# Performance work log

Hardware: AMD Instinct MI355X
Metric: run time of the kernel (lower is better)

## Reference

```python
import math
import jax, jax.numpy as jnp
import numpy as np

N, T, D, H, DH = 4, 2048, 1024, 16, 64
CAP = 30.0
EPS = 1e-5


def _layernorm(x, g, b):
    m = jnp.mean(x, axis=-1, keepdims=True)
    v = jnp.mean(jnp.square(x - m), axis=-1, keepdims=True)
    return (x - m) * jax.lax.rsqrt(v + EPS) * g + b


def _rope(x):
    # x: [N, H, t, d]; interleaved rotary (rotary-embedding-torch style), theta=10000
    t, d = x.shape[2], x.shape[3]
    inv_freq = 1.0 / (10000.0 ** (jnp.arange(0, d, 2, dtype=jnp.float32) / d))
    ang = jnp.arange(t, dtype=jnp.float32)[:, None] * inv_freq[None, :]  # [t, d/2]
    cos, sin = jnp.cos(ang), jnp.sin(ang)
    x1, x2 = x[..., 0::2], x[..., 1::2]
    r1 = x1 * cos - x2 * sin
    r2 = x1 * sin + x2 * cos
    return jnp.stack([r1, r2], axis=-1).reshape(x.shape)


def setup_inputs() -> dict:
    key = jax.random.key(0)
    ks = jax.random.split(key, 8)
    s = 0.02
    lengths = jax.random.randint(ks[6], (N,), T // 2, T + 1).astype(jnp.int32)
    key_padding_mask = jnp.arange(T)[None, :] >= lengths[:, None]  # True = pad
    attn_mask = jnp.triu(jnp.ones((T, T), dtype=bool), 1)  # causal: True = masked
    return {
        "x": jax.random.normal(ks[0], (N, T, D), jnp.float32),
        "ln_g": jnp.ones((D,), jnp.float32),
        "ln_b": jnp.zeros((D,), jnp.float32),
        "Wq": jax.random.normal(ks[1], (D, H * DH), jnp.float32) * s,
        "bq": jnp.zeros((H * DH,), jnp.float32),
        "Wk": jax.random.normal(ks[2], (D, H * DH), jnp.float32) * s,
        "bk": jnp.zeros((H * DH,), jnp.float32),
        "Wv": jax.random.normal(ks[3], (D, H * DH), jnp.float32) * s,
        "bv": jnp.zeros((H * DH,), jnp.float32),
        "Wo": jax.random.normal(ks[4], (H * DH, D), jnp.float32) * s,
        "bo": jnp.zeros((D,), jnp.float32),
        "key_padding_mask": key_padding_mask,
        "attn_mask": attn_mask,
        "key_value_sequence_lengths": lengths,
    }


def reference(x, ln_g, ln_b, Wq, bq, Wk, bk, Wv, bv, Wo, bo,
              key_padding_mask, attn_mask, key_value_sequence_lengths):
    n, t, _ = x.shape
    h = _layernorm(x, ln_g, ln_b)  # shared LN for q/k/v (self-attention)
    q = (h @ Wq + bq).reshape(n, t, H, DH).transpose(0, 2, 1, 3)  # [n,H,t,d]
    k = (h @ Wk + bk).reshape(n, t, H, DH).transpose(0, 2, 1, 3)
    v = (h @ Wv + bv).reshape(n, t, H, DH).transpose(0, 2, 1, 3)
    q = _rope(q)
    k = _rope(k)
    scores = jnp.einsum('bhtd,bhTd->bhtT', q, k) / math.sqrt(DH)
    scores = CAP * jnp.tanh(scores / CAP)  # tanh soft-cap
    mask = key_padding_mask[:, None, None, :] | attn_mask[None, None, :, :]
    scores = jnp.where(mask, -jnp.inf, scores)
    attn = jax.nn.softmax(scores, axis=-1)
    out = jnp.einsum('bhtT,bhTd->bhtd', attn, v)
    out = out.transpose(0, 2, 1, 3).reshape(n, t, H * DH)
    return out @ Wo + bo
```

## Files before the change

kernel.cpp:

```cpp
#include <hip/hip_runtime.h>
#include <hip/hip_bf16.h>

typedef unsigned short u16;
typedef unsigned int   u32;
typedef __bf16 bf16x8 __attribute__((ext_vector_type(8)));
typedef float  f32x4  __attribute__((ext_vector_type(4)));

#define NB 4
#define T_ 2048
#define D_ 1024
#define H_ 16
#define DH 64
#define M_ (NB * T_)
#define PSTR 72

__device__ __forceinline__ float bf2f(u16 u) {
    union { u32 i; float f; } v; v.i = ((u32)u) << 16; return v.f;
}
__device__ __forceinline__ u16 f2bf(float f) {
    union { float fl; u32 i; } v; v.fl = f;
    u32 r = v.i + 0x7fff + ((v.i >> 16) & 1);
    return (u16)(r >> 16);
}

__device__ __forceinline__ void gl_lds16(const u16* g, u16* l) {
    __builtin_amdgcn_global_load_lds((const __attribute__((address_space(1))) void*)g,
                                     (__attribute__((address_space(3))) void*)l,
                                     16, 0, 0);
}

__device__ __forceinline__ int detect_f32(const u16* p) {
    int weird = 0;
    const int lane = threadIdx.x & 63;
    #pragma unroll
    for (int i = 0; i < 4; ++i) {
        const u16 u = p[lane * 4 + i];
        const int e = (u >> 7) & 0xFF;
        weird += (e == 0xFF || (e >= 0x01 && e <= 0x3F) || (e >= 0xC0 && e <= 0xFE));
    }
    #pragma unroll
    for (int off = 32; off; off >>= 1) weird += __shfl_xor(weird, off);
    return weird >= 16;
}

__device__ __forceinline__ int read_len(const void* raw, int b) {
    const int* a32 = (const int*)raw;
    bool ok32 = true;
    #pragma unroll
    for (int i = 0; i < NB; ++i) {
        const int v = a32[i];
        if (v < 1 || v > T_) ok32 = false;
    }
    int v = ok32 ? a32[b] : (int)((const long long*)raw)[b];
    return min(max(v, 1), T_);
}

__global__ __launch_bounds__(256) void prep_kernel(const void* __restrict__ xraw,
                                                   const void* __restrict__ graw,
                                                   const void* __restrict__ braw,
                                                   u16* __restrict__ h,
                                                   const void* __restrict__ W0,
                                                   const void* __restrict__ W1,
                                                   const void* __restrict__ W2,
                                                   const void* __restrict__ W3,
                                                   u16* __restrict__ Wt0,
                                                   u16* __restrict__ Wt1,
                                                   u16* __restrict__ Wt2,
                                                   u16* __restrict__ Wt3,
                                                   float2* __restrict__ tab,
                                                   u32* __restrict__ ctr) {
    __shared__ __align__(16) u16 sh[64 * PSTR];
    const int bid = blockIdx.x;
    const int tid = threadIdx.x;

    if (bid < M_) {
        const int row = bid;
        const int isf = detect_f32((const u16*)xraw);
        float* red = (float*)sh;

        float xv[4];
        if (isf) {
            const float* xr = (const float*)xraw + (size_t)row * D_;
            *(float4*)xv = *(const float4*)&xr[tid * 4];
        } else {
            const u16* xr = (const u16*)xraw + (size_t)row * D_;
            u16 loc[4] __attribute__((aligned(8)));
            *(uint2*)loc = *(const uint2*)&xr[tid * 4];
            #pragma unroll
            for (int i = 0; i < 4; ++i) xv[i] = bf2f(loc[i]);
        }

        float s = xv[0] + xv[1] + xv[2] + xv[3];
        float q = xv[0]*xv[0] + xv[1]*xv[1] + xv[2]*xv[2] + xv[3]*xv[3];
        #pragma unroll
        for (int off = 32; off; off >>= 1) {
            s += __shfl_xor(s, off);
            q += __shfl_xor(q, off);
        }
        const int wave = tid >> 6, lane = tid & 63;
        if (lane == 0) { red[wave] = s; red[4 + wave] = q; }
        __syncthreads();
        s = red[0] + red[1] + red[2] + red[3];
        q = red[4] + red[5] + red[6] + red[7];

        const float mean = s * (1.0f / D_);
        const float var  = q * (1.0f / D_) - mean * mean;
        const float rs   = rsqrtf(var + 1e-5f);

        u16 o[4] __attribute__((aligned(8)));
        #pragma unroll
        for (int i = 0; i < 4; ++i) {
            const int c = tid * 4 + i;
            const float gv = isf ? ((const float*)graw)[c] : bf2f(((const u16*)graw)[c]);
            const float bv = isf ? ((const float*)braw)[c] : bf2f(((const u16*)braw)[c]);
            o[i] = f2bf((xv[i] - mean) * rs * gv + bv);
        }
        *(uint2*)&h[(size_t)row * D_ + tid * 4] = *(uint2*)o;
    } else if (bid < M_ + 1024) {
        const int w = bid - M_;
        const int z = w >> 8;
        const int t = w & 255;
        const void* Wraw = (z == 0) ? W0 : (z == 1) ? W1 : (z == 2) ? W2 : W3;
        u16* Wt          = (z == 0) ? Wt0 : (z == 1) ? Wt1 : (z == 2) ? Wt2 : Wt3;
        u16 (*tile)[PSTR] = (u16(*)[PSTR])sh;
        const int isf = detect_f32((const u16*)Wraw);
        const int n0 = (t & 15) * 64;
        const int k0 = (t >> 4) * 64;
        const int tr  = tid >> 2;
        const int tc  = (tid & 3) * 16;

        if (isf) {
            const float* W = (const float*)Wraw;
            #pragma unroll
            for (int i = 0; i < 16; ++i)
                tile[tc + i][tr] = f2bf(W[(size_t)(k0 + tr) * D_ + n0 + tc + i]);
        } else {
            const u16* W = (const u16*)Wraw;
            #pragma unroll
            for (int i = 0; i < 16; ++i)
                tile[tc + i][tr] = W[(size_t)(k0 + tr) * D_ + n0 + tc + i];
        }
        __syncthreads();
        *(uint4*)&Wt[(size_t)(n0 + tr) * D_ + k0 + tc]     = *(uint4*)&tile[tr][tc];
        *(uint4*)&Wt[(size_t)(n0 + tr) * D_ + k0 + tc + 8] = *(uint4*)&tile[tr][tc + 8];
    } else {
        const int gid = (bid - (M_ + 1024)) * 256 + tid;
        if (gid == 0 && ctr) ctr[0] = 0;
        const int t = gid >> 5, i = gid & 31;
        const float inv = exp2f(-(float)i * 0.41524101186092f);
        const float ang = (float)t * inv;
        float sv, cv;
        sincosf(ang, &sv, &cv);
        tab[gid] = make_float2(cv, sv);
    }
}

__global__ __launch_bounds__(256) void wconv_kernel(const void* __restrict__ Wraw,
                                                    u16* __restrict__ Wt) {
    __shared__ u16 tile[64][PSTR];
    const int isf = detect_f32((const u16*)Wraw);
    const int n0 = blockIdx.x * 64;
    const int k0 = blockIdx.y * 64;
    const int tid = threadIdx.x;
    const int tr  = tid >> 2;
    const int tc  = (tid & 3) * 16;

    if (isf) {
        const float* W = (const float*)Wraw;
        #pragma unroll
        for (int i = 0; i < 16; ++i)
            tile[tc + i][tr] = f2bf(W[(size_t)(k0 + tr) * D_ + n0 + tc + i]);
    } else {
        const u16* W = (const u16*)Wraw;
        #pragma unroll
        for (int i = 0; i < 16; ++i)
            tile[tc + i][tr] = W[(size_t)(k0 + tr) * D_ + n0 + tc + i];
    }
    __syncthreads();
    *(uint4*)&Wt[(size_t)(n0 + tr) * D_ + k0 + tc]     = *(uint4*)&tile[tr][tc];
    *(uint4*)&Wt[(size_t)(n0 + tr) * D_ + k0 + tc + 8] = *(uint4*)&tile[tr][tc + 8];
}

__global__ __launch_bounds__(256) void vtrans_kernel(const u16* __restrict__ vtmp,
                                                     u16* __restrict__ vt) {
    __shared__ u16 tile[64][PSTR];
    const int bh = blockIdx.y;
    const int b  = bh >> 4;
    const int hh = bh & 15;
    const int t0 = blockIdx.x * 64;
    const int tid = threadIdx.x;
    const int tr  = tid >> 2;
    const int tc  = (tid & 3) * 16;

    #pragma unroll
    for (int i = 0; i < 16; ++i)
        tile[tc + i][tr] = vtmp[(size_t)(b * T_ + t0 + tr) * D_ + hh * DH + tc + i];
    __syncthreads();
    u16* dst = vt + (size_t)bh * DH * T_ + (size_t)tr * T_ + t0;
    *(uint4*)&dst[tc]     = *(uint4*)&tile[tr][tc];
    *(uint4*)&dst[tc + 8] = *(uint4*)&tile[tr][tc + 8];
}

__global__ __launch_bounds__(256) void qkv_kernel(const u16* __restrict__ A,
                                                  const u16* __restrict__ Wt3,
                                                  const void* __restrict__ Braw,
                                                  const void* __restrict__ bqr,
                                                  const void* __restrict__ bkr,
                                                  const void* __restrict__ bvr,
                                                  u16* __restrict__ qo,
                                                  u16* __restrict__ ko,
                                                  u16* __restrict__ vo,
                                                  const float2* __restrict__ tab) {
    __shared__ __align__(16) u16 As[128 * 64];
    __shared__ __align__(16) u16 Bs[128 * 64];

    const int tid   = threadIdx.x;
    const int wave  = tid >> 6;
    const int lane  = tid & 63;
    const int quad  = lane >> 4;
    const int lr    = lane & 15;

    const int bid = blockIdx.x;
    const int wg  = (bid & 7) * 192 + (bid >> 3);
    const int ntile = (wg % 24) * 128;
    const int mtile = (wg / 24) * 128;
    const int seg   = ntile >> 10;

    const int isf = detect_f32((const u16*)Braw);

    const int srow = wave * 8 + (lane >> 3);
    const int sc   = (((lane & 7) ^ (lane >> 3)) * 8);
    const u16* aP = A   + (size_t)(mtile + srow) * D_ + sc;
    const u16* bP = Wt3 + (size_t)(ntile + srow) * D_ + sc;
    u16* aL = As + (wave * 8) * 64;
    u16* bL = Bs + (wave * 8) * 64;

    const int mbase = (wave >> 1) * 64;
    const int nbase = (wave & 1) * 64;

    f32x4 acc[4][4];
    #pragma unroll
    for (int m = 0; m < 4; ++m)
        #pragma unroll
        for (int n = 0; n < 4; ++n)
            acc[m][n] = (f32x4){0.f, 0.f, 0.f, 0.f};

    for (int k0 = 0; k0 < D_; k0 += 64) {
        #pragma unroll
        for (int j = 0; j < 4; ++j) {
            gl_lds16(aP + (size_t)(j * 32) * D_ + k0, aL + (j * 32) * 64);
            gl_lds16(bP + (size_t)(j * 32) * D_ + k0, bL + (j * 32) * 64);
        }
        __syncthreads();

        #pragma unroll
        for (int c = 0; c < 2; ++c) {
            bf16x8 af[4], bfr[4];
            #pragma unroll
            for (int m = 0; m < 4; ++m) {
                const int row = mbase + m * 16 + lr;
                af[m] = *(const bf16x8*)&As[row * 64 + (((c << 2) | quad) ^ (row & 7)) * 8];
            }
            #pragma unroll
            for (int n = 0; n < 4; ++n) {
                const int row = nbase + n * 16 + lr;
                bfr[n] = *(const bf16x8*)&Bs[row * 64 + (((c << 2) | quad) ^ (row & 7)) * 8];
            }
            #pragma unroll
            for (int m = 0; m < 4; ++m)
                #pragma unroll
                for (int n = 0; n < 4; ++n)
                    acc[m][n] = __builtin_amdgcn_mfma_f32_16x16x32_bf16(af[m], bfr[n], acc[m][n], 0, 0, 0);
        }
        __syncthreads();
    }

    const void* biasraw = (seg == 0) ? bqr : (seg == 1) ? bkr : bvr;
    u16* out            = (seg == 0) ? qo  : (seg == 1) ? ko  : vo;
    const int nloc = (ntile & 1023) + nbase;

    #pragma unroll
    for (int m = 0; m < 4; ++m) {
        #pragma unroll
        for (int n = 0; n < 4; ++n) {
            const int ncl = nloc + n * 16 + lr;
            const float bv = isf ? ((const float*)biasraw)[ncl]
                                 : bf2f(((const u16*)biasraw)[ncl]);
            #pragma unroll
            for (int r = 0; r < 4; ++r) {
                const int mrow = mtile + mbase + m * 16 + quad * 4 + r;
                float v = acc[m][n][r] + bv;
                if (seg < 2) {
                    const float other = __shfl_xor(v, 1);
                    const int d = ncl & (DH - 1);
                    const int t = mrow & (T_ - 1);
                    const float2 cs = tab[t * 32 + (d >> 1)];
                    v = (d & 1) ? (other * cs.y + v * cs.x) : (v * cs.x - other * cs.y);
                }
                out[(size_t)mrow * D_ + ncl] = f2bf(v);
            }
        }
    }
}

__global__ __launch_bounds__(256) void gemm128_kernel(const u16* __restrict__ A,
                                                      const u16* __restrict__ Bt,
                                                      const void* __restrict__ Braw,
                                                      const void* __restrict__ biasraw,
                                                      void* __restrict__ out,
                                                      const int nx,
                                                      const int mode) {
    __shared__ __align__(16) u16 As[128 * 64];
    __shared__ __align__(16) u16 Bs[128 * 64];

    const int tid   = threadIdx.x;
    const int wave  = tid >> 6;
    const int lane  = tid & 63;
    const int quad  = lane >> 4;
    const int lr    = lane & 15;

    const int bid = blockIdx.x;
    const int cpx = (nx * (M_ / 128)) >> 3;
    const int wg  = (bid & 7) * cpx + (bid >> 3);
    const int ntile = (wg % nx) * 128;
    const int mtile = (wg / nx) * 128;

    const int isf = detect_f32((const u16*)Braw);

    const int srow = wave * 8 + (lane >> 3);
    const int sc   = (((lane & 7) ^ (lane >> 3)) * 8);
    const u16* aP = A  + (size_t)(mtile + srow) * D_ + sc;
    const u16* bP = Bt + (size_t)(ntile + srow) * D_ + sc;
    u16* aL = As + (wave * 8) * 64;
    u16* bL = Bs + (wave * 8) * 64;

    const int mbase = (wave >> 1) * 64;
    const int nbase = (wave & 1) * 64;

    f32x4 acc[4][4];
    #pragma unroll
    for (int m = 0; m < 4; ++m)
        #pragma unroll
        for (int n = 0; n < 4; ++n)
            acc[m][n] = (f32x4){0.f, 0.f, 0.f, 0.f};

    for (int k0 = 0; k0 < D_; k0 += 64) {
        #pragma unroll
        for (int j = 0; j < 4; ++j) {
            gl_lds16(aP + (size_t)(j * 32) * D_ + k0, aL + (j * 32) * 64);
            gl_lds16(bP + (size_t)(j * 32) * D_ + k0, bL + (j * 32) * 64);
        }
        __syncthreads();

        #pragma unroll
        for (int c = 0; c < 2; ++c) {
            bf16x8 af[4], bfr[4];
            #pragma unroll
            for (int m = 0; m < 4; ++m) {
                const int row = mbase + m * 16 + lr;
                af[m] = *(const bf16x8*)&As[row * 64 + (((c << 2) | quad) ^ (row & 7)) * 8];
            }
            #pragma unroll
            for (int n = 0; n < 4; ++n) {
                const int row = nbase + n * 16 + lr;
                bfr[n] = *(const bf16x8*)&Bs[row * 64 + (((c << 2) | quad) ^ (row & 7)) * 8];
            }
            #pragma unroll
            for (int m = 0; m < 4; ++m)
                #pragma unroll
                for (int n = 0; n < 4; ++n)
                    acc[m][n] = __builtin_amdgcn_mfma_f32_16x16x32_bf16(af[m], bfr[n], acc[m][n], 0, 0, 0);
        }
        __syncthreads();
    }

    #pragma unroll
    for (int m = 0; m < 4; ++m) {
        #pragma unroll
        for (int n = 0; n < 4; ++n) {
            const int ncol = ntile + nbase + n * 16 + lr;
            const float bv = isf ? ((const float*)biasraw)[ncol]
                                 : bf2f(((const u16*)biasraw)[ncol]);
            #pragma unroll
            for (int r = 0; r < 4; ++r) {
                const int mrow = mtile + mbase + m * 16 + quad * 4 + r;
                float v = acc[m][n][r] + bv;
                if (mode == 2) {
                    const float other = __shfl_xor(v, 1);
                    const int d = ncol & (DH - 1);
                    const int t = mrow & (T_ - 1);
                    const int i = d >> 1;
                    const float inv = exp2f(-(float)i * 0.41524101186092f);
                    const float ang = (float)t * inv;
                    float sv, cv;
                    __sincosf(ang, &sv, &cv);
                    v = (d & 1) ? (other * sv + v * cv) : (v * cv - other * sv);
                }
                const int d  = ncol & (DH - 1);
                const int hh = ncol >> 6;
                const int t  = mrow & (T_ - 1);
                const int bb = mrow >> 11;
                if (mode == 0) {
                    if (isf) ((float*)out)[(size_t)mrow * D_ + ncol] = v;
                    else     ((u16*)out)[(size_t)mrow * D_ + ncol] = f2bf(v);
                } else if (mode == 1) {
                    ((u16*)out)[(((size_t)(bb * H_ + hh) * DH) + d) * T_ + t] = f2bf(v);
                } else {
                    ((u16*)out)[(((size_t)(bb * H_ + hh) * T_) + t) * DH + d] = f2bf(v);
                }
            }
        }
    }
}

__global__ __launch_bounds__(256) void gemm_kernel(const u16* __restrict__ A,
                                                   const void* __restrict__ Braw,
                                                   const void* __restrict__ biasraw,
                                                   void* __restrict__ out,
                                                   const int mode) {
    __shared__ __align__(16) u16 As[128 * 32];
    __shared__ __align__(16) u16 Bs[64 * 32];

    const int tid   = threadIdx.x;
    const int ntile = blockIdx.x * 64;
    const int mtile = blockIdx.y * 128;
    const int wave  = tid >> 6;
    const int lane  = tid & 63;
    const int quad  = lane >> 4;
    const int lr    = lane & 15;

    const int isf = detect_f32((const u16*)Braw);
    const float* Bf = (const float*)Braw;
    const u16*   Bu = (const u16*)Braw;

    f32x4 acc[2][4];
    #pragma unroll
    for (int s = 0; s < 2; ++s)
        #pragma unroll
        for (int n = 0; n < 4; ++n)
            acc[s][n] = (f32x4){0.f, 0.f, 0.f, 0.f};

    const int ar  = tid >> 1;
    const int akb = (tid & 1) * 16;
    const int bn  = tid & 63;
    const int bkb = (tid >> 6) * 8;
    const u16* Arow = A + (size_t)(mtile + ar) * D_ + akb;
    const size_t bcol0 = (size_t)bkb * D_ + ntile + bn;

    for (int k0 = 0; k0 < D_; k0 += 32) {
        *(uint4*)&As[ar * 32 + akb]     = *(const uint4*)(Arow + k0);
        *(uint4*)&As[ar * 32 + akb + 8] = *(const uint4*)(Arow + k0 + 8);
        {
            u16 tmp[8] __attribute__((aligned(16)));
            if (isf) {
                #pragma unroll
                for (int j = 0; j < 8; ++j) tmp[j] = f2bf(Bf[bcol0 + (size_t)(k0 + j) * D_]);
            } else {
                #pragma unroll
                for (int j = 0; j < 8; ++j) tmp[j] = Bu[bcol0 + (size_t)(k0 + j) * D_];
            }
            *(uint4*)&Bs[bn * 32 + bkb] = *(uint4*)tmp;
        }
        __syncthreads();

        const int mbase = wave * 32;
        bf16x8 af0 = *(const bf16x8*)&As[(mbase +      lr) * 32 + quad * 8];
        bf16x8 af1 = *(const bf16x8*)&As[(mbase + 16 + lr) * 32 + quad * 8];
        #pragma unroll
        for (int nt = 0; nt < 4; ++nt) {
            bf16x8 bf = *(const bf16x8*)&Bs[(nt * 16 + lr) * 32 + quad * 8];
            acc[0][nt] = __builtin_amdgcn_mfma_f32_16x16x32_bf16(af0, bf, acc[0][nt], 0, 0, 0);
            acc[1][nt] = __builtin_amdgcn_mfma_f32_16x16x32_bf16(af1, bf, acc[1][nt], 0, 0, 0);
        }
        __syncthreads();
    }

    #pragma unroll
    for (int s2 = 0; s2 < 2; ++s2) {
        #pragma unroll
        for (int nt = 0; nt < 4; ++nt) {
            const int ncol = ntile + nt * 16 + lr;
            const float bv = isf ? ((const float*)biasraw)[ncol]
                                 : bf2f(((const u16*)biasraw)[ncol]);
            #pragma unroll
            for (int r = 0; r < 4; ++r) {
                const int mrow = mtile + wave * 32 + s2 * 16 + quad * 4 + r;
                float v = acc[s2][nt][r] + bv;
                if (mode == 2) {
                    const float other = __shfl_xor(v, 1);
                    const int d = ncol & (DH - 1);
                    const int t = mrow & (T_ - 1);
                    const int i = d >> 1;
                    const float inv = exp2f(-(float)i * 0.41524101186092f);
                    const float ang = (float)t * inv;
                    const float cv = cosf(ang), sv = sinf(ang);
                    v = (d & 1) ? (other * sv + v * cv) : (v * cv - other * sv);
                }
                const int d  = ncol & (DH - 1);
                const int hh = ncol >> 6;
                const int t  = mrow & (T_ - 1);
                const int bb = mrow >> 11;
                if (mode == 0) {
                    if (isf) ((float*)out)[(size_t)mrow * D_ + ncol] = v;
                    else     ((u16*)out)[(size_t)mrow * D_ + ncol] = f2bf(v);
                } else if (mode == 1) {
                    ((u16*)out)[(((size_t)(bb * H_ + hh) * DH) + d) * T_ + t] = f2bf(v);
                } else {
                    ((u16*)out)[(((size_t)(bb * H_ + hh) * T_) + t) * DH + d] = f2bf(v);
                }
            }
        }
    }
}

__global__ __launch_bounds__(256) void attn_kernel(const u16* __restrict__ Q,
                                                   const u16* __restrict__ K,
                                                   const u16* __restrict__ Vt,
                                                   const void* __restrict__ lensraw,
                                                   u16* __restrict__ ctx,
                                                   u32* __restrict__ ctr,
                                                   const int rowmajor) {
    __shared__ __align__(16) u16 Ps[64 * PSTR];
    __shared__ __align__(16) u16 Ks[64 * PSTR];
    __shared__ __align__(16) u16 Vts[64 * PSTR];
    __shared__ int item_s;

    const int tid  = threadIdx.x;
    const int wave = tid >> 6;
    const int lane = tid & 63;
    const int quad = lane >> 4;
    const int lr   = lane & 15;
    const int srow = tid >> 2;
    const int scb  = (tid & 3) * 16;
    const int prow = wave * 16 + quad * 4;

    const float C1 = 1.44269504f / 120.0f;
    const float C2 = -60.0f * 1.44269504f;

    for (int iter = 0; ; ++iter) {
        if (tid == 0)
            item_s = ctr ? (int)atomicAdd(ctr, 1u)
                         : (iter == 0 ? (int)blockIdx.x : NB * H_ * 32);
        __syncthreads();
        const int item = item_s;
        if (item >= NB * H_ * 32) break;

        const int qt = 31 - (item >> 6);
        const int bh = item & 63;
        const int qs = qt * 64;
        const int b  = bh >> 4;
        const int hh = bh & 15;
        const int len = read_len(lensraw, b);

        const size_t qkstride = rowmajor ? (size_t)D_ : (size_t)DH;
        const size_t qkoff    = rowmajor ? ((size_t)b * T_ * D_ + hh * DH)
                                         : ((size_t)bh * T_ * DH);
        const u16* Qp = Q + qkoff;
        const u16* Kp = K + qkoff;
        const u16* Vb = Vt + (size_t)bh * DH * T_;

        *(uint4*)&Ps[srow * PSTR + scb]     = *(const uint4*)&Qp[(size_t)(qs + srow) * qkstride + scb];
        *(uint4*)&Ps[srow * PSTR + scb + 8] = *(const uint4*)&Qp[(size_t)(qs + srow) * qkstride + scb + 8];
        const bf16x8 qa0 = *(const bf16x8*)&Ps[(wave * 16 + lr) * PSTR + quad * 8];
        const bf16x8 qa1 = *(const bf16x8*)&Ps[(wave * 16 + lr) * PSTR + 32 + quad * 8];
        {
            uint4 k0 = *(const uint4*)&Kp[(size_t)srow * qkstride + scb];
            uint4 k1 = *(const uint4*)&Kp[(size_t)srow * qkstride + scb + 8];
            uint4 v0 = *(const uint4*)&Vb[(size_t)srow * T_ + scb];
            uint4 v1 = *(const uint4*)&Vb[(size_t)srow * T_ + scb + 8];
            *(uint4*)&Ks[srow * PSTR + scb]      = k0;
            *(uint4*)&Ks[srow * PSTR + scb + 8]  = k1;
            *(uint4*)&Vts[srow * PSTR + scb]     = v0;
            *(uint4*)&Vts[srow * PSTR + scb + 8] = v1;
        }
        __syncthreads();

        f32x4 acc[4];
        float l_loc[4] = {0.f, 0.f, 0.f, 0.f};
        #pragma unroll
        for (int nt = 0; nt < 4; ++nt) acc[nt] = (f32x4){0.f, 0.f, 0.f, 0.f};

        const int ktn = min(qs + 63, len - 1) / 64 + 1;

        uint4 kr0, kr1, vr0, vr1;
        for (int kt = 0; kt < ktn; ++kt) {
            const int ks = kt * 64;
            const bool havenext = (kt + 1 < ktn);

            if (havenext) {
                const int ns = ks + 64;
                kr0 = *(const uint4*)&Kp[(size_t)(ns + srow) * qkstride + scb];
                kr1 = *(const uint4*)&Kp[(size_t)(ns + srow) * qkstride + scb + 8];
                vr0 = *(const uint4*)&Vb[(size_t)srow * T_ + ns + scb];
                vr1 = *(const uint4*)&Vb[(size_t)srow * T_ + ns + scb + 8];
            }

            f32x4 s[4];
            #pragma unroll
            for (int nt = 0; nt < 4; ++nt) s[nt] = (f32x4){0.f, 0.f, 0.f, 0.f};
            __builtin_amdgcn_s_setprio(1);
            #pragma unroll
            for (int nt = 0; nt < 4; ++nt) {
                bf16x8 kb0 = *(const bf16x8*)&Ks[(nt * 16 + lr) * PSTR + quad * 8];
                bf16x8 kb1 = *(const bf16x8*)&Ks[(nt * 16 + lr) * PSTR + 32 + quad * 8];
                s[nt] = __builtin_amdgcn_mfma_f32_16x16x32_bf16(qa0, kb0, s[nt], 0, 0, 0);
                s[nt] = __builtin_amdgcn_mfma_f32_16x16x32_bf16(qa1, kb1, s[nt], 0, 0, 0);
            }
            __builtin_amdgcn_s_setprio(0);

            const bool need_mask = (ks == qs) || (ks + 63 >= len);
            if (!need_mask) {
                #pragma unroll
                for (int r = 0; r < 4; ++r) {
                    #pragma unroll
                    for (int nt = 0; nt < 4; ++nt) {
                        const float z = __builtin_amdgcn_exp2f(s[nt][r] * C1);
                        const float p = __builtin_amdgcn_exp2f(C2 * __builtin_amdgcn_rcpf(z + 1.0f));
                        l_loc[r] += p;
                        Ps[(prow + r) * PSTR + nt * 16 + lr] = f2bf(p);
                    }
                }
            } else {
                #pragma unroll
                for (int r = 0; r < 4; ++r) {
                    const int trow = qs + prow + r;
                    #pragma unroll
                    for (int nt = 0; nt < 4; ++nt) {
                        const float z = __builtin_amdgcn_exp2f(s[nt][r] * C1);
                        float p = __builtin_amdgcn_exp2f(C2 * __builtin_amdgcn_rcpf(z + 1.0f));
                        const int col = ks + nt * 16 + lr;
                        p = (col > trow || col >= len) ? 0.f : p;
                        l_loc[r] += p;
                        Ps[(prow + r) * PSTR + nt * 16 + lr] = f2bf(p);
                    }
                }
            }

            bf16x8 pa0 = *(const bf16x8*)&Ps[(wave * 16 + lr) * PSTR + quad * 8];
            bf16x8 pa1 = *(const bf16x8*)&Ps[(wave * 16 + lr) * PSTR + 32 + quad * 8];
            __builtin_amdgcn_s_setprio(1);
            #pragma unroll
            for (int nt = 0; nt < 4; ++nt) {
                bf16x8 vb0 = *(const bf16x8*)&Vts[(nt * 16 + lr) * PSTR + quad * 8];
                bf16x8 vb1 = *(const bf16x8*)&Vts[(nt * 16 + lr) * PSTR + 32 + quad * 8];
                acc[nt] = __builtin_amdgcn_mfma_f32_16x16x32_bf16(pa0, vb0, acc[nt], 0, 0, 0);
                acc[nt] = __builtin_amdgcn_mfma_f32_16x16x32_bf16(pa1, vb1, acc[nt], 0, 0, 0);
            }
            __builtin_amdgcn_s_setprio(0);

            if (havenext) {
                __syncthreads();
                *(uint4*)&Ks[srow * PSTR + scb]      = kr0;
                *(uint4*)&Ks[srow * PSTR + scb + 8]  = kr1;
                *(uint4*)&Vts[srow * PSTR + scb]     = vr0;
                *(uint4*)&Vts[srow * PSTR + scb + 8] = vr1;
                __syncthreads();
            }
        }

        #pragma unroll
        for (int r = 0; r < 4; ++r) {
            float l = l_loc[r];
            #pragma unroll
            for (int off = 1; off < 16; off <<= 1) l += __shfl_xor(l, off);
            const float invl = (l > 0.f) ? (1.0f / l) : 0.f;
            const int qrow = prow + r;
            #pragma unroll
            for (int nt = 0; nt < 4; ++nt) {
                ctx[(size_t)(b * T_ + qs + qrow) * D_ + hh * DH + nt * 16 + lr] =
                    f2bf(acc[nt][r] * invl);
            }
        }
    }
}

extern "C" void kernel_launch(void* const* d_in, const int* in_sizes, int n_in,
                              void* d_out, int out_size, void* d_ws, size_t ws_size,
                              hipStream_t stream) {
    u16* h = (u16*)d_ws;
    const size_t MD = (size_t)M_ * D_;
    const size_t WD = (size_t)D_ * D_;
    u16* q  = h + MD;
    u16* k  = q + MD;
    u16* vt = k + MD;
    const bool havewt  = ws_size >= (4 * MD + 4 * WD) * sizeof(u16);
    const bool havebig = ws_size >= (5 * MD + 4 * WD) * sizeof(u16)
                                    + (size_t)T_ * 32 * sizeof(float2) + 64;
    u16* wtq = havewt ? (vt + MD)  : nullptr;
    u16* wtk = havewt ? (wtq + WD) : nullptr;
    u16* wtv = havewt ? (wtk + WD) : nullptr;
    u16* wto = havewt ? (wtv + WD) : nullptr;
    u16* vtmp = havebig ? (wto + WD) : nullptr;
    float2* tab = havebig ? (float2*)(vtmp + MD) : nullptr;
    u32* ctr = havebig ? (u32*)(tab + (size_t)T_ * 32) : nullptr;

    if (havebig) {
        prep_kernel<<<M_ + 1024 + 256, 256, 0, stream>>>(
            d_in[0], d_in[1], d_in[2], h,
            d_in[3], d_in[5], d_in[7], d_in[9], wtq, wtk, wtv, wto, tab, ctr);

        qkv_kernel<<<1536, 256, 0, stream>>>(
            h, wtq, d_in[3], d_in[4], d_in[6], d_in[8], q, k, vtmp, tab);

        vtrans_kernel<<<dim3(T_ / 64, NB * H_), 256, 0, stream>>>(vtmp, vt);

        attn_kernel<<<1024, 256, 0, stream>>>(q, k, vt, d_in[13], h, ctr, 1);

        gemm128_kernel<<<8 * (M_ / 128), 256, 0, stream>>>(
            h, wto, d_in[9], d_in[10], d_out, 8, 0);
    } else if (havewt) {
        prep_kernel<<<M_, 256, 0, stream>>>(
            d_in[0], d_in[1], d_in[2], h,
            d_in[3], d_in[5], d_in[7], d_in[9], wtq, wtk, wtv, wto, nullptr, nullptr);
        dim3 wgrid(D_ / 64, D_ / 64);
        wconv_kernel<<<wgrid, 256, 0, stream>>>(d_in[3], wtq);
        wconv_kernel<<<wgrid, 256, 0, stream>>>(d_in[5], wtk);
        wconv_kernel<<<wgrid, 256, 0, stream>>>(d_in[7], wtv);
        wconv_kernel<<<wgrid, 256, 0, stream>>>(d_in[9], wto);

        const int g1 = 8 * (M_ / 128);
        gemm128_kernel<<<g1, 256, 0, stream>>>(h, wtq, d_in[3], d_in[4], q, 8, 2);
        gemm128_kernel<<<g1, 256, 0, stream>>>(h, wtk, d_in[5], d_in[6], k, 8, 2);
        gemm128_kernel<<<g1, 256, 0, stream>>>(h, wtv, d_in[7], d_in[8], vt, 8, 1);

        attn_kernel<<<NB * H_ * 32, 256, 0, stream>>>(q, k, vt, d_in[13], h, nullptr, 0);

        gemm128_kernel<<<g1, 256, 0, stream>>>(h, wto, d_in[9], d_in[10], d_out, 8, 0);
    } else {
        prep_kernel<<<M_, 256, 0, stream>>>(
            d_in[0], d_in[1], d_in[2], h,
            d_in[3], d_in[5], d_in[7], d_in[9], nullptr, nullptr, nullptr, nullptr, nullptr, nullptr);
        dim3 ggrid(D_ / 64, M_ / 128);
        gemm_kernel<<<ggrid, 256, 0, stream>>>(h, d_in[3], d_in[4], q, 2);
        gemm_kernel<<<ggrid, 256, 0, stream>>>(h, d_in[5], d_in[6], k, 2);
        gemm_kernel<<<ggrid, 256, 0, stream>>>(h, d_in[7], d_in[8], vt, 1);

        attn_kernel<<<NB * H_ * 32, 256, 0, stream>>>(q, k, vt, d_in[13], h, nullptr, 0);

        gemm_kernel<<<ggrid, 256, 0, stream>>>(h, d_in[9], d_in[10], d_out, 0);
    }
}
```

Measured before the change: 360.5 us.

## Double-buffer GEMM K-loop and enlarge QKV tile to 256x256

```diff
diff --git a/kernel.cpp b/kernel.cpp
--- a/kernel.cpp
+++ b/kernel.cpp
@@ -201,86 +201,94 @@
     *(uint4*)&dst[tc + 8] = *(uint4*)&tile[tr][tc + 8];
 }
 
-__global__ __launch_bounds__(256) void qkv_kernel(const u16* __restrict__ A,
-                                                  const u16* __restrict__ Wt3,
-                                                  const void* __restrict__ Braw,
-                                                  const void* __restrict__ bqr,
-                                                  const void* __restrict__ bkr,
-                                                  const void* __restrict__ bvr,
-                                                  u16* __restrict__ qo,
-                                                  u16* __restrict__ ko,
-                                                  u16* __restrict__ vo,
-                                                  const float2* __restrict__ tab) {
-    __shared__ __align__(16) u16 As[128 * 64];
-    __shared__ __align__(16) u16 Bs[128 * 64];
-
-    const int tid   = threadIdx.x;
-    const int wave  = tid >> 6;
-    const int lane  = tid & 63;
-    const int quad  = lane >> 4;
-    const int lr    = lane & 15;
+__global__ __launch_bounds__(512) void qkv256_kernel(const u16* __restrict__ A,
+                                                     const u16* __restrict__ Wt3,
+                                                     const void* __restrict__ Braw,
+                                                     const void* __restrict__ bqr,
+                                                     const void* __restrict__ bkr,
+                                                     const void* __restrict__ bvr,
+                                                     u16* __restrict__ qo,
+                                                     u16* __restrict__ ko,
+                                                     u16* __restrict__ vo,
+                                                     const float2* __restrict__ tab) {
+    __shared__ __align__(16) u16 As[2][256 * 32];
+    __shared__ __align__(16) u16 Bs[2][256 * 32];
+
+    const int tid  = threadIdx.x;
+    const int wave = tid >> 6;
+    const int lane = tid & 63;
+    const int quad = lane >> 4;
+    const int lr   = lane & 15;
+    const int wr   = wave >> 2;
+    const int wc   = wave & 3;
 
     const int bid = blockIdx.x;
-    const int wg  = (bid & 7) * 192 + (bid >> 3);
-    const int ntile = (wg % 24) * 128;
-    const int mtile = (wg / 24) * 128;
+    const int wg  = (bid & 7) * 48 + (bid >> 3);
+    const int ntile = (wg % 12) * 256;
+    const int mtile = (wg / 12) * 256;
     const int seg   = ntile >> 10;
 
     const int isf = detect_f32((const u16*)Braw);
 
-    const int srow = wave * 8 + (lane >> 3);
-    const int sc   = (((lane & 7) ^ (lane >> 3)) * 8);
-    const u16* aP = A   + (size_t)(mtile + srow) * D_ + sc;
-    const u16* bP = Wt3 + (size_t)(ntile + srow) * D_ + sc;
-    u16* aL = As + (wave * 8) * 64;
-    u16* bL = Bs + (wave * 8) * 64;
-
-    const int mbase = (wave >> 1) * 64;
-    const int nbase = (wave & 1) * 64;
-
-    f32x4 acc[4][4];
-    #pragma unroll
-    for (int m = 0; m < 4; ++m)
+    const int srow = wave * 16 + (lane >> 2);
+    const int scol = (lane & 3) * 8;
+    const u16* aP0 = A   + (size_t)(mtile + srow) * D_ + scol;
+    const u16* aP1 = A   + (size_t)(mtile + 128 + srow) * D_ + scol;
+    const u16* bP0 = Wt3 + (size_t)(ntile + srow) * D_ + scol;
+    const u16* bP1 = Wt3 + (size_t)(ntile + 128 + srow) * D_ + scol;
+    const int lo0 = (wave * 16) * 32;
+    const int lo1 = (128 + wave * 16) * 32;
+
+    f32x4 acc[8][4];
+    #pragma unroll
+    for (int m = 0; m < 8; ++m)
         #pragma unroll
         for (int n = 0; n < 4; ++n)
             acc[m][n] = (f32x4){0.f, 0.f, 0.f, 0.f};
 
-    for (int k0 = 0; k0 < D_; k0 += 64) {
-        #pragma unroll
-        for (int j = 0; j < 4; ++j) {
-            gl_lds16(aP + (size_t)(j * 32) * D_ + k0, aL + (j * 32) * 64);
-            gl_lds16(bP + (size_t)(j * 32) * D_ + k0, bL + (j * 32) * 64);
-        }
+    gl_lds16(aP0, &As[0][lo0]);
+    gl_lds16(aP1, &As[0][lo1]);
+    gl_lds16(bP0, &Bs[0][lo0]);
+    gl_lds16(bP1, &Bs[0][lo1]);
+    __syncthreads();
+
+    int cur = 0;
+    for (int kk = 0; kk < D_ / 32; ++kk) {
+        const int nxt = cur ^ 1;
+        if (kk + 1 < D_ / 32) {
+            const int k0 = (kk + 1) * 32;
+            gl_lds16(aP0 + k0, &As[nxt][lo0]);
+            gl_lds16(aP1 + k0, &As[nxt][lo1]);
+            gl_lds16(bP0 + k0, &Bs[nxt][lo0]);
+            gl_lds16(bP1 + k0, &Bs[nxt][lo1]);
+        }
+
+        bf16x8 af[8], bfr[4];
+        #pragma unroll
+        for (int m = 0; m < 8; ++m)
+            af[m] = *(const bf16x8*)&As[cur][(wr * 128 + m * 16 + lr) * 32 + quad * 8];
+        #pragma unroll
+        for (int n = 0; n < 4; ++n)
+            bfr[n] = *(const bf16x8*)&Bs[cur][(wc * 64 + n * 16 + lr) * 32 + quad * 8];
+
+        __builtin_amdgcn_s_setprio(1);
+        #pragma unroll
+        for (int m = 0; m < 8; ++m)
+            #pragma unroll
+            for (int n = 0; n < 4; ++n)
+                acc[m][n] = __builtin_amdgcn_mfma_f32_16x16x32_bf16(af[m], bfr[n], acc[m][n], 0, 0, 0);
+        __builtin_amdgcn_s_setprio(0);
+
         __syncthreads();
-
-        #pragma unroll
-        for (int c = 0; c < 2; ++c) {
-            bf16x8 af[4], bfr[4];
-            #pragma unroll
-            for (int m = 0; m < 4; ++m) {
-                const int row = mbase + m * 16 + lr;
-                af[m] = *(const bf16x8*)&As[row * 64 + (((c << 2) | quad) ^ (row & 7)) * 8];
-            }
-            #pragma unroll
-            for (int n = 0; n < 4; ++n) {
-                const int row = nbase + n * 16 + lr;
-                bfr[n] = *(const bf16x8*)&Bs[row * 64 + (((c << 2) | quad) ^ (row & 7)) * 8];
-            }
-            #pragma unroll
-            for (int m = 0; m < 4; ++m)
-                #pragma unroll
-                for (int n = 0; n < 4; ++n)
-                    acc[m][n] = __builtin_amdgcn_mfma_f32_16x16x32_bf16(af[m], bfr[n], acc[m][n], 0, 0, 0);
-        }
-        __syncthreads();
+        cur = nxt;
     }
 
     const void* biasraw = (seg == 0) ? bqr : (seg == 1) ? bkr : bvr;
     u16* out            = (seg == 0) ? qo  : (seg == 1) ? ko  : vo;
-    const int nloc = (ntile & 1023) + nbase;
-
-    #pragma unroll
-    for (int m = 0; m < 4; ++m) {
+    const int nloc = (ntile & 1023) + wc * 64;
+
+    #pragma unroll
+    for (int m = 0; m < 8; ++m) {
         #pragma unroll
         for (int n = 0; n < 4; ++n) {
             const int ncl = nloc + n * 16 + lr;
@@ -288,7 +296,7 @@
                                  : bf2f(((const u16*)biasraw)[ncl]);
             #pragma unroll
             for (int r = 0; r < 4; ++r) {
-                const int mrow = mtile + mbase + m * 16 + quad * 4 + r;
+                const int mrow = mtile + wr * 128 + m * 16 + quad * 4 + r;
                 float v = acc[m][n][r] + bv;
                 if (seg < 2) {
                     const float other = __shfl_xor(v, 1);
@@ -310,8 +318,8 @@
                                                       void* __restrict__ out,
                                                       const int nx,
                                                       const int mode) {
-    __shared__ __align__(16) u16 As[128 * 64];
-    __shared__ __align__(16) u16 Bs[128 * 64];
+    __shared__ __align__(16) u16 As[2][128 * 32];
+    __shared__ __align__(16) u16 Bs[2][128 * 32];
 
     const int tid   = threadIdx.x;
     const int wave  = tid >> 6;
@@ -327,12 +335,14 @@
 
     const int isf = detect_f32((const u16*)Braw);
 
-    const int srow = wave * 8 + (lane >> 3);
-    const int sc   = (((lane & 7) ^ (lane >> 3)) * 8);
-    const u16* aP = A  + (size_t)(mtile + srow) * D_ + sc;
-    const u16* bP = Bt + (size_t)(ntile + srow) * D_ + sc;
-    u16* aL = As + (wave * 8) * 64;
-    u16* bL = Bs + (wave * 8) * 64;
+    const int srow = wave * 16 + (lane >> 2);
+    const int scol = (lane & 3) * 8;
+    const u16* aP0 = A  + (size_t)(mtile + srow) * D_ + scol;
+    const u16* aP1 = A  + (size_t)(mtile + 64 + srow) * D_ + scol;
+    const u16* bP0 = Bt + (size_t)(ntile + srow) * D_ + scol;
+    const u16* bP1 = Bt + (size_t)(ntile + 64 + srow) * D_ + scol;
+    const int lo0 = (wave * 16) * 32;
+    const int lo1 = (64 + wave * 16) * 32;
 
     const int mbase = (wave >> 1) * 64;
     const int nbase = (wave & 1) * 64;
@@ -344,34 +354,41 @@
         for (int n = 0; n < 4; ++n)
             acc[m][n] = (f32x4){0.f, 0.f, 0.f, 0.f};
 
-    for (int k0 = 0; k0 < D_; k0 += 64) {
-        #pragma unroll
-        for (int j = 0; j < 4; ++j) {
-            gl_lds16(aP + (size_t)(j * 32) * D_ + k0, aL + (j * 32) * 64);
-            gl_lds16(bP + (size_t)(j * 32) * D_ + k0, bL + (j * 32) * 64);
-        }
+    gl_lds16(aP0, &As[0][lo0]);
+    gl_lds16(aP1, &As[0][lo1]);
+    gl_lds16(bP0, &Bs[0][lo0]);
+    gl_lds16(bP1, &Bs[0][lo1]);
+    __syncthreads();
+
+    int cur = 0;
+    for (int kk = 0; kk < D_ / 32; ++kk) {
+        const int nxt = cur ^ 1;
+        if (kk + 1 < D_ / 32) {
+            const int k0 = (kk + 1) * 32;
+            gl_lds16(aP0 + k0, &As[nxt][lo0]);
+            gl_lds16(aP1 + k0, &As[nxt][lo1]);
+            gl_lds16(bP0 + k0, &Bs[nxt][lo0]);
+            gl_lds16(bP1 + k0, &Bs[nxt][lo1]);
+        }
+
+        bf16x8 af[4], bfr[4];
+        #pragma unroll
+        for (int m = 0; m < 4; ++m)
+            af[m] = *(const bf16x8*)&As[cur][(mbase + m * 16 + lr) * 32 + quad * 8];
+        #pragma unroll
+        for (int n = 0; n < 4; ++n)
+            bfr[n] = *(const bf16x8*)&Bs[cur][(nbase + n * 16 + lr) * 32 + quad * 8];
+
+        __builtin_amdgcn_s_setprio(1);
+        #pragma unroll
+        for (int m = 0; m < 4; ++m)
+            #pragma unroll
+            for (int n = 0; n < 4; ++n)
+                acc[m][n] = __builtin_amdgcn_mfma_f32_16x16x32_bf16(af[m], bfr[n], acc[m][n], 0, 0, 0);
+        __builtin_amdgcn_s_setprio(0);
+
         __syncthreads();
-
-        #pragma unroll
-        for (int c = 0; c < 2; ++c) {
-            bf16x8 af[4], bfr[4];
-            #pragma unroll
-            for (int m = 0; m < 4; ++m) {
-                const int row = mbase + m * 16 + lr;
-                af[m] = *(const bf16x8*)&As[row * 64 + (((c << 2) | quad) ^ (row & 7)) * 8];
-            }
-            #pragma unroll
-            for (int n = 0; n < 4; ++n) {
-                const int row = nbase + n * 16 + lr;
-                bfr[n] = *(const bf16x8*)&Bs[row * 64 + (((c << 2) | quad) ^ (row & 7)) * 8];
-            }
-            #pragma unroll
-            for (int m = 0; m < 4; ++m)
-                #pragma unroll
-                for (int n = 0; n < 4; ++n)
-                    acc[m][n] = __builtin_amdgcn_mfma_f32_16x16x32_bf16(af[m], bfr[n], acc[m][n], 0, 0, 0);
-        }
-        __syncthreads();
+        cur = nxt;
     }
 
     #pragma unroll
@@ -699,7 +716,7 @@
             d_in[0], d_in[1], d_in[2], h,
             d_in[3], d_in[5], d_in[7], d_in[9], wtq, wtk, wtv, wto, tab, ctr);
 
-        qkv_kernel<<<1536, 256, 0, stream>>>(
+        qkv256_kernel<<<384, 512, 0, stream>>>(
             h, wtq, d_in[3], d_in[4], d_in[6], d_in[8], q, k, vtmp, tab);
 
         vtrans_kernel<<<dim3(T_ / 64, NB * H_), 256, 0, stream>>>(vtmp, vt);
```

After: 397.4 us. 1.1x slower.

## Double-buffer LDS tiles in QKV and output GEMMs to overlap loads with MFMA

Applied to the files above, without the earlier changes.

```diff
diff --git a/kernel.cpp b/kernel.cpp
--- a/kernel.cpp
+++ b/kernel.cpp
@@ -211,8 +211,8 @@
                                                   u16* __restrict__ ko,
                                                   u16* __restrict__ vo,
                                                   const float2* __restrict__ tab) {
-    __shared__ __align__(16) u16 As[128 * 64];
-    __shared__ __align__(16) u16 Bs[128 * 64];
+    __shared__ __align__(16) u16 As[2][128 * 64];
+    __shared__ __align__(16) u16 Bs[2][128 * 64];
 
     const int tid   = threadIdx.x;
     const int wave  = tid >> 6;
@@ -232,8 +232,7 @@
     const int sc   = (((lane & 7) ^ (lane >> 3)) * 8);
     const u16* aP = A   + (size_t)(mtile + srow) * D_ + sc;
     const u16* bP = Wt3 + (size_t)(ntile + srow) * D_ + sc;
-    u16* aL = As + (wave * 8) * 64;
-    u16* bL = Bs + (wave * 8) * 64;
+    const int lofs = (wave * 8) * 64;
 
     const int mbase = (wave >> 1) * 64;
     const int nbase = (wave & 1) * 64;
@@ -245,13 +244,24 @@
         for (int n = 0; n < 4; ++n)
             acc[m][n] = (f32x4){0.f, 0.f, 0.f, 0.f};
 
-    for (int k0 = 0; k0 < D_; k0 += 64) {
-        #pragma unroll
-        for (int j = 0; j < 4; ++j) {
-            gl_lds16(aP + (size_t)(j * 32) * D_ + k0, aL + (j * 32) * 64);
-            gl_lds16(bP + (size_t)(j * 32) * D_ + k0, bL + (j * 32) * 64);
-        }
-        __syncthreads();
+    #pragma unroll
+    for (int j = 0; j < 4; ++j) {
+        gl_lds16(aP + (size_t)(j * 32) * D_, &As[0][lofs + (j * 32) * 64]);
+        gl_lds16(bP + (size_t)(j * 32) * D_, &Bs[0][lofs + (j * 32) * 64]);
+    }
+    __syncthreads();
+
+    int cur = 0;
+    for (int kk = 0; kk < D_ / 64; ++kk) {
+        const int nxt = cur ^ 1;
+        if (kk + 1 < D_ / 64) {
+            const int k0 = (kk + 1) * 64;
+            #pragma unroll
+            for (int j = 0; j < 4; ++j) {
+                gl_lds16(aP + (size_t)(j * 32) * D_ + k0, &As[nxt][lofs + (j * 32) * 64]);
+                gl_lds16(bP + (size_t)(j * 32) * D_ + k0, &Bs[nxt][lofs + (j * 32) * 64]);
+            }
+        }
 
         #pragma unroll
         for (int c = 0; c < 2; ++c) {
@@ -259,20 +269,24 @@
             #pragma unroll
             for (int m = 0; m < 4; ++m) {
                 const int row = mbase + m * 16 + lr;
-                af[m] = *(const bf16x8*)&As[row * 64 + (((c << 2) | quad) ^ (row & 7)) * 8];
+                af[m] = *(const bf16x8*)&As[cur][row * 64 + (((c << 2) | quad) ^ (row & 7)) * 8];
             }
             #pragma unroll
             for (int n = 0; n < 4; ++n) {
                 const int row = nbase + n * 16 + lr;
-                bfr[n] = *(const bf16x8*)&Bs[row * 64 + (((c << 2) | quad) ^ (row & 7)) * 8];
-            }
+                bfr[n] = *(const bf16x8*)&Bs[cur][row * 64 + (((c << 2) | quad) ^ (row & 7)) * 8];
+            }
+            __builtin_amdgcn_s_setprio(1);
             #pragma unroll
             for (int m = 0; m < 4; ++m)
                 #pragma unroll
                 for (int n = 0; n < 4; ++n)
                     acc[m][n] = __builtin_amdgcn_mfma_f32_16x16x32_bf16(af[m], bfr[n], acc[m][n], 0, 0, 0);
-        }
+            __builtin_amdgcn_s_setprio(0);
+        }
+
         __syncthreads();
+        cur = nxt;
     }
 
     const void* biasraw = (seg == 0) ? bqr : (seg == 1) ? bkr : bvr;
@@ -310,8 +324,8 @@
                                                       void* __restrict__ out,
                                                       const int nx,
                                                       const int mode) {
-    __shared__ __align__(16) u16 As[128 * 64];
-    __shared__ __align__(16) u16 Bs[128 * 64];
+    __shared__ __align__(16) u16 As[2][128 * 64];
+    __shared__ __align__(16) u16 Bs[2][128 * 64];
 
     const int tid   = threadIdx.x;
     const int wave  = tid >> 6;
@@ -331,8 +345,7 @@
     const int sc   = (((lane & 7) ^ (lane >> 3)) * 8);
     const u16* aP = A  + (size_t)(mtile + srow) * D_ + sc;
     const u16* bP = Bt + (size_t)(ntile + srow) * D_ + sc;
-    u16* aL = As + (wave * 8) * 64;
-    u16* bL = Bs + (wave * 8) * 64;
+    const int lofs = (wave * 8) * 64;
 
     const int mbase = (wave >> 1) * 64;
     const int nbase = (wave & 1) * 64;
@@ -344,13 +357,24 @@
         for (int n = 0; n < 4; ++n)
             acc[m][n] = (f32x4){0.f, 0.f, 0.f, 0.f};
 
-    for (int k0 = 0; k0 < D_; k0 += 64) {
-        #pragma unroll
-        for (int j = 0; j < 4; ++j) {
-            gl_lds16(aP + (size_t)(j * 32) * D_ + k0, aL + (j * 32) * 64);
-            gl_lds16(bP + (size_t)(j * 32) * D_ + k0, bL + (j * 32) * 64);
-        }
-        __syncthreads();
+    #pragma unroll
+    for (int j = 0; j < 4; ++j) {
+        gl_lds16(aP + (size_t)(j * 32) * D_, &As[0][lofs + (j * 32) * 64]);
+        gl_lds16(bP + (size_t)(j * 32) * D_, &Bs[0][lofs + (j * 32) * 64]);
+    }
+    __syncthreads();
+
+    int cur = 0;
+    for (int kk = 0; kk < D_ / 64; ++kk) {
+        const int nxt = cur ^ 1;
+        if (kk + 1 < D_ / 64) {
+            const int k0 = (kk + 1) * 64;
+            #pragma unroll
+            for (int j = 0; j < 4; ++j) {
+                gl_lds16(aP + (size_t)(j * 32) * D_ + k0, &As[nxt][lofs + (j * 32) * 64]);
+                gl_lds16(bP + (size_t)(j * 32) * D_ + k0, &Bs[nxt][lofs + (j * 32) * 64]);
+            }
+        }
 
         #pragma unroll
         for (int c = 0; c < 2; ++c) {
@@ -358,20 +382,24 @@
             #pragma unroll
             for (int m = 0; m < 4; ++m) {
                 const int row = mbase + m * 16 + lr;
-                af[m] = *(const bf16x8*)&As[row * 64 + (((c << 2) | quad) ^ (row & 7)) * 8];
+                af[m] = *(const bf16x8*)&As[cur][row * 64 + (((c << 2) | quad) ^ (row & 7)) * 8];
             }
             #pragma unroll
             for (int n = 0; n < 4; ++n) {
                 const int row = nbase + n * 16 + lr;
-                bfr[n] = *(const bf16x8*)&Bs[row * 64 + (((c << 2) | quad) ^ (row & 7)) * 8];
-            }
+                bfr[n] = *(const bf16x8*)&Bs[cur][row * 64 + (((c << 2) | quad) ^ (row & 7)) * 8];
+            }
+            __builtin_amdgcn_s_setprio(1);
             #pragma unroll
             for (int m = 0; m < 4; ++m)
                 #pragma unroll
                 for (int n = 0; n < 4; ++n)
                     acc[m][n] = __builtin_amdgcn_mfma_f32_16x16x32_bf16(af[m], bfr[n], acc[m][n], 0, 0, 0);
-        }
+            __builtin_amdgcn_s_setprio(0);
+        }
+
         __syncthreads();
+        cur = nxt;
     }
 
     #pragma unroll
```

Result: no change. 366.2 us (+1.6%).

## Triple-buffer GEMM K-loop with async global-to-LDS prefetch and single barrier

Applied to the files above, without the earlier changes.

```diff
diff --git a/kernel.cpp b/kernel.cpp
--- a/kernel.cpp
+++ b/kernel.cpp
@@ -201,6 +201,14 @@
     *(uint4*)&dst[tc + 8] = *(uint4*)&tile[tr][tc + 8];
 }
 
+#define STAGE3(As_, Bs_, buf, aPg, bPg, k0, lofs)                                   \
+    do {                                                                            \
+        gl_lds16((aPg) + (k0),                 &(As_)[buf][(lofs)]);                \
+        gl_lds16((aPg) + 16 * D_ + (k0),       &(As_)[buf][(lofs) + 16 * 32]);      \
+        gl_lds16((bPg) + (k0),                 &(Bs_)[buf][(lofs)]);                \
+        gl_lds16((bPg) + 16 * D_ + (k0),       &(Bs_)[buf][(lofs) + 16 * 32]);      \
+    } while (0)
+
 __global__ __launch_bounds__(256) void qkv_kernel(const u16* __restrict__ A,
                                                   const u16* __restrict__ Wt3,
                                                   const void* __restrict__ Braw,
@@ -211,8 +219,8 @@
                                                   u16* __restrict__ ko,
                                                   u16* __restrict__ vo,
                                                   const float2* __restrict__ tab) {
-    __shared__ __align__(16) u16 As[128 * 64];
-    __shared__ __align__(16) u16 Bs[128 * 64];
+    __shared__ __align__(16) u16 As[3][128 * 32];
+    __shared__ __align__(16) u16 Bs[3][128 * 32];
 
     const int tid   = threadIdx.x;
     const int wave  = tid >> 6;
@@ -228,15 +236,15 @@
 
     const int isf = detect_f32((const u16*)Braw);
 
-    const int srow = wave * 8 + (lane >> 3);
-    const int sc   = (((lane & 7) ^ (lane >> 3)) * 8);
-    const u16* aP = A   + (size_t)(mtile + srow) * D_ + sc;
-    const u16* bP = Wt3 + (size_t)(ntile + srow) * D_ + sc;
-    u16* aL = As + (wave * 8) * 64;
-    u16* bL = Bs + (wave * 8) * 64;
+    const int sr  = lane >> 2;
+    const int scw = 8 * ((lane & 3) ^ ((lane >> 3) & 3));
+    const u16* aPg = A   + (size_t)(mtile + wave * 32 + sr) * D_ + scw;
+    const u16* bPg = Wt3 + (size_t)(ntile + wave * 32 + sr) * D_ + scw;
+    const int lofs = (wave * 32) * 32;
 
     const int mbase = (wave >> 1) * 64;
     const int nbase = (wave & 1) * 64;
+    const int ksl   = (quad ^ ((lr >> 1) & 3)) * 8;
 
     f32x4 acc[4][4];
     #pragma unroll
@@ -245,34 +253,36 @@
         for (int n = 0; n < 4; ++n)
             acc[m][n] = (f32x4){0.f, 0.f, 0.f, 0.f};
 
-    for (int k0 = 0; k0 < D_; k0 += 64) {
-        #pragma unroll
-        for (int j = 0; j < 4; ++j) {
-            gl_lds16(aP + (size_t)(j * 32) * D_ + k0, aL + (j * 32) * 64);
-            gl_lds16(bP + (size_t)(j * 32) * D_ + k0, bL + (j * 32) * 64);
-        }
-        __syncthreads();
-
-        #pragma unroll
-        for (int c = 0; c < 2; ++c) {
-            bf16x8 af[4], bfr[4];
-            #pragma unroll
-            for (int m = 0; m < 4; ++m) {
-                const int row = mbase + m * 16 + lr;
-                af[m] = *(const bf16x8*)&As[row * 64 + (((c << 2) | quad) ^ (row & 7)) * 8];
-            }
-            #pragma unroll
-            for (int n = 0; n < 4; ++n) {
-                const int row = nbase + n * 16 + lr;
-                bfr[n] = *(const bf16x8*)&Bs[row * 64 + (((c << 2) | quad) ^ (row & 7)) * 8];
-            }
-            #pragma unroll
-            for (int m = 0; m < 4; ++m)
-                #pragma unroll
-                for (int n = 0; n < 4; ++n)
-                    acc[m][n] = __builtin_amdgcn_mfma_f32_16x16x32_bf16(af[m], bfr[n], acc[m][n], 0, 0, 0);
-        }
-        __syncthreads();
+    STAGE3(As, Bs, 0, aPg, bPg, 0, lofs);
+    STAGE3(As, Bs, 1, aPg, bPg, 32, lofs);
+    asm volatile("s_waitcnt vmcnt(4)" ::: "memory");
+    __builtin_amdgcn_s_barrier();
+
+    int b0 = 0, b1 = 1, b2 = 2;
+    for (int kk = 0; kk < 32; ++kk) {
+        if (kk + 2 < 32) STAGE3(As, Bs, b2, aPg, bPg, (kk + 2) * 32, lofs);
+
+        bf16x8 af[4], bfr[4];
+        #pragma unroll
+        for (int m = 0; m < 4; ++m)
+            af[m] = *(const bf16x8*)&As[b0][(mbase + m * 16 + lr) * 32 + ksl];
+        #pragma unroll
+        for (int n = 0; n < 4; ++n)
+            bfr[n] = *(const bf16x8*)&Bs[b0][(nbase + n * 16 + lr) * 32 + ksl];
+
+        __builtin_amdgcn_s_setprio(1);
+        #pragma unroll
+        for (int m = 0; m < 4; ++m)
+            #pragma unroll
+            for (int n = 0; n < 4; ++n)
+                acc[m][n] = __builtin_amdgcn_mfma_f32_16x16x32_bf16(af[m], bfr[n], acc[m][n], 0, 0, 0);
+        __builtin_amdgcn_s_setprio(0);
+
+        if (kk < 30) asm volatile("s_waitcnt vmcnt(4)" ::: "memory");
+        else         asm volatile("s_waitcnt vmcnt(0)" ::: "memory");
+        __builtin_amdgcn_s_barrier();
+
+        const int t = b0; b0 = b1; b1 = b2; b2 = t;
     }
 
     const void* biasraw = (seg == 0) ? bqr : (seg == 1) ? bkr : bvr;
@@ -310,8 +320,8 @@
                                                       void* __restrict__ out,
                                                       const int nx,
                                                       const int mode) {
-    __shared__ __align__(16) u16 As[128 * 64];
-    __shared__ __align__(16) u16 Bs[128 * 64];
+    __shared__ __align__(16) u16 As[3][128 * 32];
+    __shared__ __align__(16) u16 Bs[3][128 * 32];
 
     const int tid   = threadIdx.x;
     const int wave  = tid >> 6;
@@ -327,15 +337,15 @@
 
     const int isf = detect_f32((const u16*)Braw);
 
-    const int srow = wave * 8 + (lane >> 3);
-    const int sc   = (((lane & 7) ^ (lane >> 3)) * 8);
-    const u16* aP = A  + (size_t)(mtile + srow) * D_ + sc;
-    const u16* bP = Bt + (size_t)(ntile + srow) * D_ + sc;
-    u16* aL = As + (wave * 8) * 64;
-    u16* bL = Bs + (wave * 8) * 64;
+    const int sr  = lane >> 2;
+    const int scw = 8 * ((lane & 3) ^ ((lane >> 3) & 3));
+    const u16* aPg = A  + (size_t)(mtile + wave * 32 + sr) * D_ + scw;
+    const u16* bPg = Bt + (size_t)(ntile + wave * 32 + sr) * D_ + scw;
+    const int lofs = (wave * 32) * 32;
 
     const int mbase = (wave >> 1) * 64;
     const int nbase = (wave & 1) * 64;
+    const int ksl   = (quad ^ ((lr >> 1) & 3)) * 8;
 
     f32x4 acc[4][4];
     #pragma unroll
@@ -344,34 +354,36 @@
         for (int n = 0; n < 4; ++n)
             acc[m][n] = (f32x4){0.f, 0.f, 0.f, 0.f};
 
-    for (int k0 = 0; k0 < D_; k0 += 64) {
-        #pragma unroll
-        for (int j = 0; j < 4; ++j) {
-            gl_lds16(aP + (size_t)(j * 32) * D_ + k0, aL + (j * 32) * 64);
-            gl_lds16(bP + (size_t)(j * 32) * D_ + k0, bL + (j * 32) * 64);
-        }
-        __syncthreads();
-
-        #pragma unroll
-        for (int c = 0; c < 2; ++c) {
-            bf16x8 af[4], bfr[4];
-            #pragma unroll
-            for (int m = 0; m < 4; ++m) {
-                const int row = mbase + m * 16 + lr;
-                af[m] = *(const bf16x8*)&As[row * 64 + (((c << 2) | quad) ^ (row & 7)) * 8];
-            }
-            #pragma unroll
-            for (int n = 0; n < 4; ++n) {
-                const int row = nbase + n * 16 + lr;
-                bfr[n] = *(const bf16x8*)&Bs[row * 64 + (((c << 2) | quad) ^ (row & 7)) * 8];
-            }
-            #pragma unroll
-            for (int m = 0; m < 4; ++m)
-                #pragma unroll
-                for (int n = 0; n < 4; ++n)
-                    acc[m][n] = __builtin_amdgcn_mfma_f32_16x16x32_bf16(af[m], bfr[n], acc[m][n], 0, 0, 0);
-        }
-        __syncthreads();
+    STAGE3(As, Bs, 0, aPg, bPg, 0, lofs);
+    STAGE3(As, Bs, 1, aPg, bPg, 32, lofs);
+    asm volatile("s_waitcnt vmcnt(4)" ::: "memory");
+    __builtin_amdgcn_s_barrier();
+
+    int b0 = 0, b1 = 1, b2 = 2;
+    for (int kk = 0; kk < 32; ++kk) {
+        if (kk + 2 < 32) STAGE3(As, Bs, b2, aPg, bPg, (kk + 2) * 32, lofs);
+
+        bf16x8 af[4], bfr[4];
+        #pragma unroll
+        for (int m = 0; m < 4; ++m)
+            af[m] = *(const bf16x8*)&As[b0][(mbase + m * 16 + lr) * 32 + ksl];
+        #pragma unroll
+        for (int n = 0; n < 4; ++n)
+            bfr[n] = *(const bf16x8*)&Bs[b0][(nbase + n * 16 + lr) * 32 + ksl];
+
+        __builtin_amdgcn_s_setprio(1);
+        #pragma unroll
+        for (int m = 0; m < 4; ++m)
+            #pragma unroll
+            for (int n = 0; n < 4; ++n)
+                acc[m][n] = __builtin_amdgcn_mfma_f32_16x16x32_bf16(af[m], bfr[n], acc[m][n], 0, 0, 0);
+        __builtin_amdgcn_s_setprio(0);
+
+        if (kk < 30) asm volatile("s_waitcnt vmcnt(4)" ::: "memory");
+        else         asm volatile("s_waitcnt vmcnt(0)" ::: "memory");
+        __builtin_amdgcn_s_barrier();
+
+        const int t = b0; b0 = b1; b1 = b2; b2 = t;
     }
 
     #pragma unroll
```

Result: faster. 350.2 us (-2.9%).
